# Kernel optimization log

Measured on AMD Instinct MI355X. Metric: run time of the kernel, lower is better.

The kernel has to match this reference:

```python
import jax, jax.numpy as jnp
import numpy as np

B, S, D, A = 32, 2048, 512, 256


def setup_inputs() -> dict:
    key = jax.random.key(0)
    ks = jax.random.split(key, 9)
    enc = jax.random.normal(ks[0], (B, S, D), dtype=jnp.float32)
    dec = jax.random.normal(ks[1], (B, 1, D), dtype=jnp.float32)
    prev = jax.random.uniform(ks[2], (B, S), dtype=jnp.float32)
    prev = prev / jnp.sum(prev, axis=1, keepdims=True)  # normalized prev attention
    noise = jax.random.normal(ks[3], (B, S), dtype=jnp.float32)
    W = jax.random.normal(ks[4], (A, D), dtype=jnp.float32) / np.sqrt(D)
    V = jax.random.normal(ks[5], (A, D), dtype=jnp.float32) / np.sqrt(D)
    b = jax.random.normal(ks[6], (A,), dtype=jnp.float32)
    v_w = jax.random.normal(ks[7], (1, A), dtype=jnp.float32)
    v_g = jnp.full((1,), np.sqrt(1.0 / A), dtype=jnp.float32)  # weight_norm g init
    v_bias = jax.random.normal(ks[8], (1,), dtype=jnp.float32)
    r = jnp.full((1,), -4.0, dtype=jnp.float32)
    return {"encoder_outputs": enc, "decoder_h": dec, "prev_alpha": prev,
            "noise": noise, "W": W, "V": V, "b": b, "v_w": v_w,
            "v_g": v_g, "v_bias": v_bias, "r": r}


def reference(encoder_outputs, decoder_h, prev_alpha, noise, W, V, b, v_w, v_g, v_bias, r):
    # Energy: tanh-MLP Bahdanau score with weight-normed output projection
    h = jnp.tanh(jnp.einsum('bsd,ad->bsa', encoder_outputs, W)
                 + jnp.einsum('bod,ad->boa', decoder_h, V)  # [B,1,A] broadcasts over S
                 + b)
    w_eff = v_g * v_w / jnp.linalg.norm(v_w)       # weight_norm: g * v / ||v||
    energy = jnp.einsum('bsa,oa->bso', h, w_eff)[..., 0] + v_bias[0] + r[0]  # [B,S]
    # Soft monotonic attention recurrence
    p_select = jax.nn.sigmoid(energy + noise)
    log1mp = jnp.log(jnp.clip(1.0 - p_select, 1e-10, 1.0))
    cumprod_1mp = jnp.exp(jnp.cumsum(log1mp, axis=1))  # safe_cumprod
    alpha = p_select * cumprod_1mp * jnp.cumsum(prev_alpha / cumprod_1mp, axis=1)
    # Context: enc^T @ alpha
    context = jnp.einsum('bsd,bs->bd', encoder_outputs, alpha)
    return context, alpha
```

## Files before the change

kernel.cpp:

```cpp
#include <hip/hip_runtime.h>
#include <math.h>

#define B_  32
#define S_  2048
#define D_  512
#define A_  256
#define BS_ (B_ * S_)

#define WEFF_OFF  0
#define DEC_OFF   256
#define EPART_OFF 8448
#define CTX_OFF   (8448 + BS_)

typedef _Float16 f16x8 __attribute__((ext_vector_type(8)));
typedef __fp16   fp16x2 __attribute__((ext_vector_type(2)));
typedef _Float16 half4 __attribute__((ext_vector_type(4)));
typedef float floatx4 __attribute__((ext_vector_type(4)));

__device__ __forceinline__ void glds16(const void* g, void* l) {
    __builtin_amdgcn_global_load_lds(
        (const __attribute__((address_space(1))) void*)g,
        (__attribute__((address_space(3))) void*)l, 16, 0, 0);
}

__global__ void ma_prep_kernel(const float* __restrict__ v_w,
                               const float* __restrict__ v_g,
                               const float* __restrict__ dec,
                               const float* __restrict__ V,
                               const float* __restrict__ bvec,
                               const float* __restrict__ W,
                               _Float16* __restrict__ W16,
                               float* __restrict__ ws) {
    __shared__ float sh[D_];
    const int bid = blockIdx.x, t = threadIdx.x;
    if (bid == 0) {
        float v = v_w[t];
        float sq = v * v;
        #pragma unroll
        for (int off = 32; off > 0; off >>= 1) sq += __shfl_down(sq, off, 64);
        if ((t & 63) == 0) sh[t >> 6] = sq;
        __syncthreads();
        float n2 = sh[0] + sh[1] + sh[2] + sh[3];
        ws[WEFF_OFF + t] = v_g[0] * v / sqrtf(n2);
    } else if (bid <= B_) {
        const int b = bid - 1;
        sh[t]       = dec[b * D_ + t];
        sh[t + 256] = dec[b * D_ + 256 + t];
        __syncthreads();
        const float4* Vr = (const float4*)(V + (size_t)t * D_);
        float acc = 0.f;
        #pragma unroll 4
        for (int k = 0; k < D_ / 4; ++k) {
            float4 v4 = Vr[k];
            acc = fmaf(v4.x, sh[4*k+0], acc);
            acc = fmaf(v4.y, sh[4*k+1], acc);
            acc = fmaf(v4.z, sh[4*k+2], acc);
            acc = fmaf(v4.w, sh[4*k+3], acc);
        }
        ws[DEC_OFF + b * A_ + t] = acc + bvec[t];
    } else {
        int i = (bid - (B_ + 1)) * 256 + t;
        float4 v = ((const float4*)W)[i];
        half4 h;
        h[0] = (_Float16)v.x; h[1] = (_Float16)v.y;
        h[2] = (_Float16)v.z; h[3] = (_Float16)v.w;
        ((half4*)W16)[i] = h;
    }
}

__global__ __launch_bounds__(512) void ma_energy_mfma(
        const float* __restrict__ enc,
        const _Float16* __restrict__ W16,
        const float* __restrict__ ws_in,
        float* __restrict__ energy) {
    __shared__ __align__(16) float    As[2][128 * 32];
    __shared__ __align__(16) _Float16 Bs[2][256 * 32];
    __shared__ float red[4][128];

    const int t  = threadIdx.x;
    const int bx = blockIdx.x;
    const size_t R0 = (size_t)bx * 128;
    const int batch = bx >> 4;

    const int lane = t & 63, wid = t >> 6;
    const int wm = wid >> 2, wn = wid & 3;
    const int fr = lane & 15, kq = lane >> 4;

    const int arow = t >> 3, ac = t & 7;
    const float* AgS0 = enc + (R0 + (size_t)arow) * D_ + (ac ^ (arow & 7)) * 4;
    const float* AgS1 = AgS0 + (size_t)64 * D_;
    const int brow = t >> 2, bc = t & 3;
    const _Float16* BgS0 = W16 + (size_t)brow * D_ + (bc ^ ((brow >> 1) & 3)) * 8;
    const _Float16* BgS1 = BgS0 + (size_t)128 * D_;

    const int axc0 = ((2 * kq)     ^ (fr & 7)) * 4;
    const int axc1 = ((2 * kq + 1) ^ (fr & 7)) * 4;
    const int bxo  = (kq ^ ((fr >> 1) & 3)) * 8;

    floatx4 acc[4][4];
    #pragma unroll
    for (int m = 0; m < 4; ++m)
        #pragma unroll
        for (int n = 0; n < 4; ++n) acc[m][n] = (floatx4)0.f;

    glds16(AgS0, &As[0][wid * 256]);
    glds16(AgS1, &As[0][wid * 256 + 2048]);
    glds16(BgS0, &Bs[0][wid * 512]);
    glds16(BgS1, &Bs[0][wid * 512 + 4096]);
    __syncthreads();

    #pragma unroll 1
    for (int kt = 0; kt < 16; ++kt) {
        const int cur = kt & 1;
        if (kt < 15) {
            const int nxt = cur ^ 1;
            const int ko = (kt + 1) * 32;
            glds16(AgS0 + ko, &As[nxt][wid * 256]);
            glds16(AgS1 + ko, &As[nxt][wid * 256 + 2048]);
            glds16(BgS0 + ko, &Bs[nxt][wid * 512]);
            glds16(BgS1 + ko, &Bs[nxt][wid * 512 + 4096]);
        }
        f16x8 af[4];
        #pragma unroll
        for (int m = 0; m < 4; ++m) {
            const int rbase = (wm * 64 + m * 16 + fr) * 32;
            float4 lo = *(const float4*)&As[cur][rbase + axc0];
            float4 hi = *(const float4*)&As[cur][rbase + axc1];
            union { fp16x2 h2[4]; f16x8 v; } u;
            u.h2[0] = __builtin_amdgcn_cvt_pkrtz(lo.x, lo.y);
            u.h2[1] = __builtin_amdgcn_cvt_pkrtz(lo.z, lo.w);
            u.h2[2] = __builtin_amdgcn_cvt_pkrtz(hi.x, hi.y);
            u.h2[3] = __builtin_amdgcn_cvt_pkrtz(hi.z, hi.w);
            af[m] = u.v;
        }
        f16x8 bf[4];
        #pragma unroll
        for (int n = 0; n < 4; ++n)
            bf[n] = *(const f16x8*)&Bs[cur][(wn * 64 + n * 16 + fr) * 32 + bxo];
        #pragma unroll
        for (int m = 0; m < 4; ++m)
            #pragma unroll
            for (int n = 0; n < 4; ++n)
                acc[m][n] = __builtin_amdgcn_mfma_f32_16x16x32_f16(af[m], bf[n], acc[m][n], 0, 0, 0);
        __syncthreads();
    }

    const float* weff  = ws_in + WEFF_OFF;
    const float* dterm = ws_in + DEC_OFF + batch * A_;
    float wj[4], dj[4];
    #pragma unroll
    for (int n = 0; n < 4; ++n) {
        int a = wn * 64 + n * 16 + fr;
        wj[n] = weff[a];
        dj[n] = dterm[a];
    }
    #pragma unroll
    for (int m = 0; m < 4; ++m) {
        #pragma unroll
        for (int r = 0; r < 4; ++r) {
            float v = 0.f;
            #pragma unroll
            for (int n = 0; n < 4; ++n) {
                float x = acc[m][n][r] + dj[n];
                float e = __expf(2.f * x);
                v += (1.f - 2.f / (e + 1.f)) * wj[n];
            }
            #pragma unroll
            for (int mask = 1; mask < 16; mask <<= 1)
                v += __shfl_xor(v, mask, 64);
            if (fr == 0)
                red[wn][wm * 64 + m * 16 + (kq << 2) + r] = v;
        }
    }
    __syncthreads();
    if (t < 128)
        energy[R0 + t] = red[0][t] + red[1][t] + red[2][t] + red[3][t];
}

__global__ void ma_scan_kernel(const float* __restrict__ energy,
                               const float* __restrict__ noise,
                               const float* __restrict__ prev,
                               const float* __restrict__ v_bias,
                               const float* __restrict__ r,
                               float* __restrict__ alpha_out) {
    int b = blockIdx.x, t = threadIdx.x;
    const float bias = v_bias[0] + r[0];
    int base = b * S_ + t * 8;
    float p[8], av[8], bv[8];
    #pragma unroll
    for (int i = 0; i < 8; ++i) {
        float e = energy[base + i] + bias + noise[base + i];
        float pi = 1.f / (1.f + expf(-e));
        p[i]  = pi;
        av[i] = fmaxf(1.f - pi, 1e-10f);
        bv[i] = prev[base + i];
    }
    float Ai = 1.f, Bi = 0.f;
    #pragma unroll
    for (int i = 0; i < 8; ++i) { Bi = av[i] * Bi + bv[i]; Ai *= av[i]; }
    int lane = t & 63;
    #pragma unroll
    for (int off = 1; off < 64; off <<= 1) {
        float Ap = __shfl_up(Ai, off, 64);
        float Bp = __shfl_up(Bi, off, 64);
        if (lane >= off) { Bi = Ai * Bp + Bi; Ai = Ai * Ap; }
    }
    __shared__ float wA[4], wB[4];
    int w = t >> 6;
    if (lane == 63) { wA[w] = Ai; wB[w] = Bi; }
    __syncthreads();
    float Ax = __shfl_up(Ai, 1, 64);
    float Bx = __shfl_up(Bi, 1, 64);
    if (lane == 0) { Ax = 1.f; Bx = 0.f; }
    float PwA = 1.f, PwB = 0.f;
    for (int q = 0; q < w; ++q) { PwB = wA[q] * PwB + wB[q]; PwA *= wA[q]; }
    float T = Ax * PwB + Bx;
    #pragma unroll
    for (int i = 0; i < 8; ++i) {
        T = av[i] * T + bv[i];
        alpha_out[base + i] = p[i] * T;
    }
}

__global__ void ma_ctxpart_kernel(const float* __restrict__ enc,
                                  const float* __restrict__ alpha,
                                  float* __restrict__ cpart) {
    int b = blockIdx.x, sc = blockIdx.y, t = threadIdx.x;
    const float* e0 = enc + ((size_t)b * S_ + sc * 64) * D_;
    const float* al = alpha + b * S_ + sc * 64;
    float a0 = 0.f, a1 = 0.f;
    for (int s = 0; s < 64; ++s) {
        float avv = al[s];
        a0 = fmaf(e0[(size_t)s * D_ + t], avv, a0);
        a1 = fmaf(e0[(size_t)s * D_ + 256 + t], avv, a1);
    }
    cpart[((size_t)(sc * B_ + b)) * D_ + t]       = a0;
    cpart[((size_t)(sc * B_ + b)) * D_ + 256 + t] = a1;
}

__global__ void ma_ctxreduce_kernel(const float* __restrict__ cpart,
                                    float* __restrict__ ctx) {
    int b = blockIdx.x, t = threadIdx.x;
    #pragma unroll
    for (int h = 0; h < 2; ++h) {
        int d = t + h * 256;
        float s = 0.f;
        #pragma unroll
        for (int q = 0; q < 32; ++q) s += cpart[((size_t)(q * B_ + b)) * D_ + d];
        ctx[b * D_ + d] = s;
    }
}

extern "C" void kernel_launch(void* const* d_in, const int* in_sizes, int n_in,
                              void* d_out, int out_size, void* d_ws, size_t ws_size,
                              hipStream_t stream) {
    const float* enc    = (const float*)d_in[0];
    const float* dec    = (const float*)d_in[1];
    const float* prev   = (const float*)d_in[2];
    const float* noise  = (const float*)d_in[3];
    const float* W      = (const float*)d_in[4];
    const float* V      = (const float*)d_in[5];
    const float* bvec   = (const float*)d_in[6];
    const float* v_w    = (const float*)d_in[7];
    const float* v_g    = (const float*)d_in[8];
    const float* v_bias = (const float*)d_in[9];
    const float* r      = (const float*)d_in[10];

    float* out = (float*)d_out;
    float* ws  = (float*)d_ws;
    float* alpha = out + B_ * D_;
    _Float16* W16 = (_Float16*)(ws + CTX_OFF);

    ma_prep_kernel<<<1 + B_ + 128, 256, 0, stream>>>(v_w, v_g, dec, V, bvec, W, W16, ws);
    ma_energy_mfma<<<512, 512, 0, stream>>>(enc, W16, ws, ws + EPART_OFF);
    ma_scan_kernel<<<B_, 256, 0, stream>>>(ws + EPART_OFF, noise, prev, v_bias, r, alpha);
    dim3 gc(B_, 32);
    ma_ctxpart_kernel<<<gc, 256, 0, stream>>>(enc, alpha, ws + CTX_OFF);
    ma_ctxreduce_kernel<<<B_, 256, 0, stream>>>(ws + CTX_OFF, out);
}
```

Baseline: 77.83 us.

## Triple-buffer A tiles with deeper prefetch in energy GEMM; vectorize context partial sums

The energy MFMA kernel moves from double buffering to three A stages and two B stages in one shared buffer, issuing loads two or three k-tiles ahead. It uses explicit vmcnt waits and raw barriers in place of __syncthreads, so waves keep multiple global-to-LDS loads in flight and stall less on memory latency. The context partial kernel now reads float4 and splits the 64 rows between two thread halves, combining them through shared memory. In exchange, LDS use rises to 80 KB per block, which may limit occupancy, and the hand-written wait counts are fragile.

```diff
diff --git a/kernel.cpp b/kernel.cpp
--- a/kernel.cpp
+++ b/kernel.cpp
@@ -73,9 +73,9 @@
         const _Float16* __restrict__ W16,
         const float* __restrict__ ws_in,
         float* __restrict__ energy) {
-    __shared__ __align__(16) float    As[2][128 * 32];
-    __shared__ __align__(16) _Float16 Bs[2][256 * 32];
-    __shared__ float red[4][128];
+    __shared__ __align__(16) char smem[81920];
+    float*    const Asm = (float*)smem;
+    _Float16* const Bsm = (_Float16*)(smem + 49152);
 
     const int t  = threadIdx.x;
     const int bx = blockIdx.x;
@@ -103,48 +103,74 @@
         #pragma unroll
         for (int n = 0; n < 4; ++n) acc[m][n] = (floatx4)0.f;
 
-    glds16(AgS0, &As[0][wid * 256]);
-    glds16(AgS1, &As[0][wid * 256 + 2048]);
-    glds16(BgS0, &Bs[0][wid * 512]);
-    glds16(BgS1, &Bs[0][wid * 512 + 4096]);
+#define STAGE_A(kt, buf) do { \
+        glds16(AgS0 + (kt) * 32, Asm + (buf) * 4096 + wid * 256); \
+        glds16(AgS1 + (kt) * 32, Asm + (buf) * 4096 + wid * 256 + 2048); } while (0)
+#define STAGE_B(kt, buf) do { \
+        glds16(BgS0 + (kt) * 32, Bsm + (buf) * 8192 + wid * 512); \
+        glds16(BgS1 + (kt) * 32, Bsm + (buf) * 8192 + wid * 512 + 4096); } while (0)
+
+#define COMPUTE(ca, cb) do { \
+        const float*    Abuf = Asm + (ca) * 4096; \
+        const _Float16* Bbuf = Bsm + (cb) * 8192; \
+        f16x8 af[4], bf[4]; \
+        _Pragma("unroll") \
+        for (int m = 0; m < 4; ++m) { \
+            const int rbase = (wm * 64 + m * 16 + fr) * 32; \
+            float4 lo = *(const float4*)&Abuf[rbase + axc0]; \
+            float4 hi = *(const float4*)&Abuf[rbase + axc1]; \
+            union { fp16x2 h2[4]; f16x8 v; } u; \
+            u.h2[0] = __builtin_amdgcn_cvt_pkrtz(lo.x, lo.y); \
+            u.h2[1] = __builtin_amdgcn_cvt_pkrtz(lo.z, lo.w); \
+            u.h2[2] = __builtin_amdgcn_cvt_pkrtz(hi.x, hi.y); \
+            u.h2[3] = __builtin_amdgcn_cvt_pkrtz(hi.z, hi.w); \
+            af[m] = u.v; \
+        } \
+        _Pragma("unroll") \
+        for (int n = 0; n < 4; ++n) \
+            bf[n] = *(const f16x8*)&Bbuf[(wn * 64 + n * 16 + fr) * 32 + bxo]; \
+        _Pragma("unroll") \
+        for (int m = 0; m < 4; ++m) \
+            _Pragma("unroll") \
+            for (int n = 0; n < 4; ++n) \
+                acc[m][n] = __builtin_amdgcn_mfma_f32_16x16x32_f16(af[m], bf[n], acc[m][n], 0, 0, 0); \
+    } while (0)
+
+    STAGE_A(0, 0); STAGE_B(0, 0);
+    STAGE_A(1, 1); STAGE_B(1, 1);
+    STAGE_A(2, 2);
+    asm volatile("s_waitcnt vmcnt(6)" ::: "memory");
+    __builtin_amdgcn_s_barrier();
+    __builtin_amdgcn_sched_barrier(0);
+
+    int ca = 0, cb = 0;
+    #pragma unroll 1
+    for (int kt = 0; kt < 13; ++kt) {
+        COMPUTE(ca, cb);
+        __builtin_amdgcn_s_barrier();
+        STAGE_B(kt + 2, cb);
+        STAGE_A(kt + 3, ca);
+        asm volatile("s_waitcnt vmcnt(6)" ::: "memory");
+        __builtin_amdgcn_s_barrier();
+        __builtin_amdgcn_sched_barrier(0);
+        ca = (ca == 2) ? 0 : ca + 1;
+        cb ^= 1;
+    }
+    COMPUTE(1, 1);
+    __builtin_amdgcn_s_barrier();
+    STAGE_B(15, 1);
+    asm volatile("s_waitcnt vmcnt(4)" ::: "memory");
+    __builtin_amdgcn_s_barrier();
+    __builtin_amdgcn_sched_barrier(0);
+    COMPUTE(2, 0);
+    __builtin_amdgcn_s_barrier();
+    asm volatile("s_waitcnt vmcnt(0)" ::: "memory");
+    __builtin_amdgcn_s_barrier();
+    __builtin_amdgcn_sched_barrier(0);
+    COMPUTE(0, 1);
     __syncthreads();
 
-    #pragma unroll 1
-    for (int kt = 0; kt < 16; ++kt) {
-        const int cur = kt & 1;
-        if (kt < 15) {
-            const int nxt = cur ^ 1;
-            const int ko = (kt + 1) * 32;
-            glds16(AgS0 + ko, &As[nxt][wid * 256]);
-            glds16(AgS1 + ko, &As[nxt][wid * 256 + 2048]);
-            glds16(BgS0 + ko, &Bs[nxt][wid * 512]);
-            glds16(BgS1 + ko, &Bs[nxt][wid * 512 + 4096]);
-        }
-        f16x8 af[4];
-        #pragma unroll
-        for (int m = 0; m < 4; ++m) {
-            const int rbase = (wm * 64 + m * 16 + fr) * 32;
-            float4 lo = *(const float4*)&As[cur][rbase + axc0];
-            float4 hi = *(const float4*)&As[cur][rbase + axc1];
-            union { fp16x2 h2[4]; f16x8 v; } u;
-            u.h2[0] = __builtin_amdgcn_cvt_pkrtz(lo.x, lo.y);
-            u.h2[1] = __builtin_amdgcn_cvt_pkrtz(lo.z, lo.w);
-            u.h2[2] = __builtin_amdgcn_cvt_pkrtz(hi.x, hi.y);
-            u.h2[3] = __builtin_amdgcn_cvt_pkrtz(hi.z, hi.w);
-            af[m] = u.v;
-        }
-        f16x8 bf[4];
-        #pragma unroll
-        for (int n = 0; n < 4; ++n)
-            bf[n] = *(const f16x8*)&Bs[cur][(wn * 64 + n * 16 + fr) * 32 + bxo];
-        #pragma unroll
-        for (int m = 0; m < 4; ++m)
-            #pragma unroll
-            for (int n = 0; n < 4; ++n)
-                acc[m][n] = __builtin_amdgcn_mfma_f32_16x16x32_f16(af[m], bf[n], acc[m][n], 0, 0, 0);
-        __syncthreads();
-    }
-
+    float* const red = (float*)smem;
     const float* weff  = ws_in + WEFF_OFF;
     const float* dterm = ws_in + DEC_OFF + batch * A_;
     float wj[4], dj[4];
@@ -169,12 +195,15 @@
             for (int mask = 1; mask < 16; mask <<= 1)
                 v += __shfl_xor(v, mask, 64);
             if (fr == 0)
-                red[wn][wm * 64 + m * 16 + (kq << 2) + r] = v;
+                red[wn * 128 + wm * 64 + m * 16 + (kq << 2) + r] = v;
         }
     }
     __syncthreads();
     if (t < 128)
-        energy[R0 + t] = red[0][t] + red[1][t] + red[2][t] + red[3][t];
+        energy[R0 + t] = red[t] + red[128 + t] + red[256 + t] + red[384 + t];
+#undef STAGE_A
+#undef STAGE_B
+#undef COMPUTE
 }
 
 __global__ void ma_scan_kernel(const float* __restrict__ energy,
@@ -226,16 +255,28 @@
                                   const float* __restrict__ alpha,
                                   float* __restrict__ cpart) {
     int b = blockIdx.x, sc = blockIdx.y, t = threadIdx.x;
-    const float* e0 = enc + ((size_t)b * S_ + sc * 64) * D_;
+    const int sp = t >> 7;
+    const int d4 = t & 127;
+    const float4* e = (const float4*)(enc + ((size_t)b * S_ + sc * 64) * D_);
     const float* al = alpha + b * S_ + sc * 64;
-    float a0 = 0.f, a1 = 0.f;
-    for (int s = 0; s < 64; ++s) {
-        float avv = al[s];
-        a0 = fmaf(e0[(size_t)s * D_ + t], avv, a0);
-        a1 = fmaf(e0[(size_t)s * D_ + 256 + t], avv, a1);
-    }
-    cpart[((size_t)(sc * B_ + b)) * D_ + t]       = a0;
-    cpart[((size_t)(sc * B_ + b)) * D_ + 256 + t] = a1;
+    float4 acc = {0.f, 0.f, 0.f, 0.f};
+    #pragma unroll 4
+    for (int s = sp; s < 64; s += 2) {
+        float a = al[s];
+        float4 v = e[(size_t)s * 128 + d4];
+        acc.x = fmaf(v.x, a, acc.x);
+        acc.y = fmaf(v.y, a, acc.y);
+        acc.z = fmaf(v.z, a, acc.z);
+        acc.w = fmaf(v.w, a, acc.w);
+    }
+    __shared__ float4 sh[128];
+    if (sp == 1) sh[d4] = acc;
+    __syncthreads();
+    if (sp == 0) {
+        float4 o = sh[d4];
+        acc.x += o.x; acc.y += o.y; acc.z += o.z; acc.w += o.w;
+        ((float4*)(cpart + ((size_t)(sc * B_ + b)) * D_))[d4] = acc;
+    }
 }
 
 __global__ void ma_ctxreduce_kernel(const float* __restrict__ cpart,
```

Measured after the change: 78.28 us. Within noise of the previous version (+0.6%).

## Retile energy GEMM to 64-row blocks with fp16 LDS staging; vectorize context partial sums

Applied to the files above, without the earlier changes.

The energy MFMA kernel moves from 128x256 tiles with 512 threads and double-buffered fp32 A tiles to 64x256 tiles with 256 threads. A is converted to fp16 in registers before being stored to LDS, K steps are 64 wide, and the kernel is single-buffered with two barriers per step. This halves LDS footprint so four blocks can share a CU, and it removes the repeated per-MFMA A conversions, at the cost of losing overlap between loads and compute. The context partial kernel now uses float4 loads, splits S across two thread halves and combines them through shared memory, which widens memory transactions.

```diff
diff --git a/kernel.cpp b/kernel.cpp
--- a/kernel.cpp
+++ b/kernel.cpp
@@ -68,34 +68,30 @@
     }
 }
 
-__global__ __launch_bounds__(512) void ma_energy_mfma(
+__global__ __launch_bounds__(256, 4) void ma_energy_mfma(
         const float* __restrict__ enc,
         const _Float16* __restrict__ W16,
         const float* __restrict__ ws_in,
         float* __restrict__ energy) {
-    __shared__ __align__(16) float    As[2][128 * 32];
-    __shared__ __align__(16) _Float16 Bs[2][256 * 32];
-    __shared__ float red[4][128];
+    __shared__ __align__(16) _Float16 As[64 * 64];
+    __shared__ __align__(16) _Float16 Bs[256 * 64];
 
     const int t  = threadIdx.x;
     const int bx = blockIdx.x;
-    const size_t R0 = (size_t)bx * 128;
-    const int batch = bx >> 4;
+    const size_t R0 = (size_t)bx * 64;
+    const int batch = bx >> 5;
 
     const int lane = t & 63, wid = t >> 6;
-    const int wm = wid >> 2, wn = wid & 3;
     const int fr = lane & 15, kq = lane >> 4;
 
-    const int arow = t >> 3, ac = t & 7;
-    const float* AgS0 = enc + (R0 + (size_t)arow) * D_ + (ac ^ (arow & 7)) * 4;
-    const float* AgS1 = AgS0 + (size_t)64 * D_;
-    const int brow = t >> 2, bc = t & 3;
-    const _Float16* BgS0 = W16 + (size_t)brow * D_ + (bc ^ ((brow >> 1) & 3)) * 8;
-    const _Float16* BgS1 = BgS0 + (size_t)128 * D_;
-
-    const int axc0 = ((2 * kq)     ^ (fr & 7)) * 4;
-    const int axc1 = ((2 * kq + 1) ^ (fr & 7)) * 4;
-    const int bxo  = (kq ^ ((fr >> 1) & 3)) * 8;
+    const int ar = t & 63, akc = t >> 6;
+    const float* Ag = enc + (R0 + (size_t)ar) * D_ + akc * 16;
+    _Float16* const As_w0 = &As[ar * 64 + (((2 * akc)     ^ (ar & 7)) * 8)];
+    _Float16* const As_w1 = &As[ar * 64 + (((2 * akc + 1) ^ (ar & 7)) * 8)];
+
+    const int brg = lane >> 3, bch = lane & 7;
+    const _Float16* Bg = W16 + (size_t)(wid * 64 + brg) * D_ + (bch ^ brg) * 8;
+    _Float16* const Bdst = &Bs[wid * 4096];
 
     floatx4 acc[4][4];
     #pragma unroll
@@ -103,54 +99,67 @@
         #pragma unroll
         for (int n = 0; n < 4; ++n) acc[m][n] = (floatx4)0.f;
 
-    glds16(AgS0, &As[0][wid * 256]);
-    glds16(AgS1, &As[0][wid * 256 + 2048]);
-    glds16(BgS0, &Bs[0][wid * 512]);
-    glds16(BgS1, &Bs[0][wid * 512 + 4096]);
+#define STAGE(kt) do { \
+        _Pragma("unroll") \
+        for (int j = 0; j < 8; ++j) \
+            glds16(Bg + (kt) * 64 + (size_t)j * 8 * D_, Bdst + j * 512); \
+        float4 v0 = *(const float4*)(Ag + (kt) * 64); \
+        float4 v1 = *(const float4*)(Ag + (kt) * 64 + 4); \
+        float4 v2 = *(const float4*)(Ag + (kt) * 64 + 8); \
+        float4 v3 = *(const float4*)(Ag + (kt) * 64 + 12); \
+        union { fp16x2 h2[4]; f16x8 v; } u0, u1; \
+        u0.h2[0] = __builtin_amdgcn_cvt_pkrtz(v0.x, v0.y); \
+        u0.h2[1] = __builtin_amdgcn_cvt_pkrtz(v0.z, v0.w); \
+        u0.h2[2] = __builtin_amdgcn_cvt_pkrtz(v1.x, v1.y); \
+        u0.h2[3] = __builtin_amdgcn_cvt_pkrtz(v1.z, v1.w); \
+        u1.h2[0] = __builtin_amdgcn_cvt_pkrtz(v2.x, v2.y); \
+        u1.h2[1] = __builtin_amdgcn_cvt_pkrtz(v2.z, v2.w); \
+        u1.h2[2] = __builtin_amdgcn_cvt_pkrtz(v3.x, v3.y); \
+        u1.h2[3] = __builtin_amdgcn_cvt_pkrtz(v3.z, v3.w); \
+        *(f16x8*)As_w0 = u0.v; \
+        *(f16x8*)As_w1 = u1.v; \
+    } while (0)
+
+    STAGE(0);
     __syncthreads();
 
     #pragma unroll 1
-    for (int kt = 0; kt < 16; ++kt) {
-        const int cur = kt & 1;
-        if (kt < 15) {
-            const int nxt = cur ^ 1;
-            const int ko = (kt + 1) * 32;
-            glds16(AgS0 + ko, &As[nxt][wid * 256]);
-            glds16(AgS1 + ko, &As[nxt][wid * 256 + 2048]);
-            glds16(BgS0 + ko, &Bs[nxt][wid * 512]);
-            glds16(BgS1 + ko, &Bs[nxt][wid * 512 + 4096]);
+    for (int kt = 0; kt < 8; ++kt) {
+        #pragma unroll
+        for (int ks = 0; ks < 2; ++ks) {
+            f16x8 af[4], bf[4];
+            const int csw = ks * 4 + kq;
+            #pragma unroll
+            for (int m = 0; m < 4; ++m) {
+                const int row = m * 16 + fr;
+                af[m] = *(const f16x8*)&As[row * 64 + ((csw ^ (row & 7)) * 8)];
+            }
+            #pragma unroll
+            for (int n = 0; n < 4; ++n) {
+                const int row = wid * 64 + n * 16 + fr;
+                bf[n] = *(const f16x8*)&Bs[row * 64 + ((csw ^ (row & 7)) * 8)];
+            }
+            #pragma unroll
+            for (int m = 0; m < 4; ++m)
+                #pragma unroll
+                for (int n = 0; n < 4; ++n)
+                    acc[m][n] = __builtin_amdgcn_mfma_f32_16x16x32_f16(af[m], bf[n], acc[m][n], 0, 0, 0);
         }
-        f16x8 af[4];
-        #pragma unroll
-        for (int m = 0; m < 4; ++m) {
-            const int rbase = (wm * 64 + m * 16 + fr) * 32;
-            float4 lo = *(const float4*)&As[cur][rbase + axc0];
-            float4 hi = *(const float4*)&As[cur][rbase + axc1];
-            union { fp16x2 h2[4]; f16x8 v; } u;
-            u.h2[0] = __builtin_amdgcn_cvt_pkrtz(lo.x, lo.y);
-            u.h2[1] = __builtin_amdgcn_cvt_pkrtz(lo.z, lo.w);
-            u.h2[2] = __builtin_amdgcn_cvt_pkrtz(hi.x, hi.y);
-            u.h2[3] = __builtin_amdgcn_cvt_pkrtz(hi.z, hi.w);
-            af[m] = u.v;
+        __syncthreads();
+        if (kt < 7) {
+            STAGE(kt + 1);
+            __syncthreads();
         }
-        f16x8 bf[4];
-        #pragma unroll
-        for (int n = 0; n < 4; ++n)
-            bf[n] = *(const f16x8*)&Bs[cur][(wn * 64 + n * 16 + fr) * 32 + bxo];
-        #pragma unroll
-        for (int m = 0; m < 4; ++m)
-            #pragma unroll
-            for (int n = 0; n < 4; ++n)
-                acc[m][n] = __builtin_amdgcn_mfma_f32_16x16x32_f16(af[m], bf[n], acc[m][n], 0, 0, 0);
-        __syncthreads();
-    }
-
+    }
+#undef STAGE
+
+    float* const red = (float*)As;
     const float* weff  = ws_in + WEFF_OFF;
     const float* dterm = ws_in + DEC_OFF + batch * A_;
     float wj[4], dj[4];
     #pragma unroll
     for (int n = 0; n < 4; ++n) {
-        int a = wn * 64 + n * 16 + fr;
+        int a = wid * 64 + n * 16 + fr;
         wj[n] = weff[a];
         dj[n] = dterm[a];
     }
@@ -169,12 +178,12 @@
             for (int mask = 1; mask < 16; mask <<= 1)
                 v += __shfl_xor(v, mask, 64);
             if (fr == 0)
-                red[wn][wm * 64 + m * 16 + (kq << 2) + r] = v;
+                red[wid * 64 + m * 16 + (kq << 2) + r] = v;
         }
     }
     __syncthreads();
-    if (t < 128)
-        energy[R0 + t] = red[0][t] + red[1][t] + red[2][t] + red[3][t];
+    if (t < 64)
+        energy[R0 + t] = red[t] + red[64 + t] + red[128 + t] + red[192 + t];
 }
 
 __global__ void ma_scan_kernel(const float* __restrict__ energy,
@@ -226,16 +235,28 @@
                                   const float* __restrict__ alpha,
                                   float* __restrict__ cpart) {
     int b = blockIdx.x, sc = blockIdx.y, t = threadIdx.x;
-    const float* e0 = enc + ((size_t)b * S_ + sc * 64) * D_;
+    const int sp = t >> 7;
+    const int d4 = t & 127;
+    const float4* e = (const float4*)(enc + ((size_t)b * S_ + sc * 64) * D_);
     const float* al = alpha + b * S_ + sc * 64;
-    float a0 = 0.f, a1 = 0.f;
-    for (int s = 0; s < 64; ++s) {
-        float avv = al[s];
-        a0 = fmaf(e0[(size_t)s * D_ + t], avv, a0);
-        a1 = fmaf(e0[(size_t)s * D_ + 256 + t], avv, a1);
-    }
-    cpart[((size_t)(sc * B_ + b)) * D_ + t]       = a0;
-    cpart[((size_t)(sc * B_ + b)) * D_ + 256 + t] = a1;
+    float4 acc = {0.f, 0.f, 0.f, 0.f};
+    #pragma unroll 4
+    for (int s = sp; s < 64; s += 2) {
+        float a = al[s];
+        float4 v = e[(size_t)s * 128 + d4];
+        acc.x = fmaf(v.x, a, acc.x);
+        acc.y = fmaf(v.y, a, acc.y);
+        acc.z = fmaf(v.z, a, acc.z);
+        acc.w = fmaf(v.w, a, acc.w);
+    }
+    __shared__ float4 sh[128];
+    if (sp == 1) sh[d4] = acc;
+    __syncthreads();
+    if (sp == 0) {
+        float4 o = sh[d4];
+        acc.x += o.x; acc.y += o.y; acc.z += o.z; acc.w += o.w;
+        ((float4*)(cpart + ((size_t)(sc * B_ + b)) * D_))[d4] = acc;
+    }
 }
 
 __global__ void ma_ctxreduce_kernel(const float* __restrict__ cpart,
@@ -272,7 +293,7 @@
     _Float16* W16 = (_Float16*)(ws + CTX_OFF);
 
     ma_prep_kernel<<<1 + B_ + 128, 256, 0, stream>>>(v_w, v_g, dec, V, bvec, W, W16, ws);
-    ma_energy_mfma<<<512, 512, 0, stream>>>(enc, W16, ws, ws + EPART_OFF);
+    ma_energy_mfma<<<1024, 256, 0, stream>>>(enc, W16, ws, ws + EPART_OFF);
     ma_scan_kernel<<<B_, 256, 0, stream>>>(ws + EPART_OFF, noise, prev, v_bias, r, alpha);
     dim3 gc(B_, 32);
     ma_ctxpart_kernel<<<gc, 256, 0, stream>>>(enc, alpha, ws + CTX_OFF);
```

New measurement: 85.07 us. 1.09x slower.
